# Kernel optimization log

Hardware: AMD Instinct MI355X
Metric: run time of the kernel (lower is better)

## Reference

```python
import jax, jax.numpy as jnp
import numpy as np

NEIGHBOUR_NUM = 8  # args.neighbour_num


def _sqrdis_map(x, y):
    # x: [B,M,3], y: [B,N,3] -> [B,M,N] squared distances
    x2 = jnp.sum(x * x, axis=-1)
    y2 = jnp.sum(y * y, axis=-1)
    inner = jnp.einsum('bmd,bnd->bmn', x, y)
    return x2[:, :, None] + y2[:, None, :] - 2.0 * inner


def _chamfer(x, y):
    d = _sqrdis_map(x, y)
    return d.min(axis=2), d.min(axis=1)


def _neighbor_index(v, k):
    # torch.topk(dist, k+1, largest=False) then drop self
    d = _sqrdis_map(v, v)
    idx = jax.lax.top_k(-d, k + 1)[1]  # ascending distance order
    return idx[:, :, 1:]


def _arap(idx, dp, sp):
    B = dp.shape[0]
    bid = jnp.arange(B)[:, None, None]
    dn = dp[bid, idx] - dp[:, :, None, :]  # [B,N,K,3]
    sn = sp[bid, idx] - sp[:, :, None, :]
    dd = jnp.sqrt(jnp.sum(dn * dn, axis=-1) + 1e-5)
    sd = jnp.sqrt(jnp.sum(sn * sn, axis=-1) + 1e-5)
    diff = dd - sd
    return jnp.sum(diff * diff) / B


def setup_inputs() -> dict:
    key = jax.random.key(0)
    ks = jax.random.split(key, 7)
    T, B, N = 3, 4, 4096
    return {
        'phi': jax.random.normal(ks[0], (T, B, 1024), dtype=jnp.float32),
        'point_weight': jax.random.normal(ks[1], (T, B, N, 1), dtype=jnp.float32),
        'deform_rigid_points': 0.5 * jax.random.normal(ks[2], (T, B, N, 3), dtype=jnp.float32),
        'deformation_points': 0.5 * jax.random.normal(ks[3], (T, B, N, 3), dtype=jnp.float32),
        'rigid_matrix': 0.1 * jax.random.normal(ks[4], (T, B, 4, 4), dtype=jnp.float32),
        'source_points': jax.random.uniform(ks[5], (B, N, 3), dtype=jnp.float32, minval=-1.0, maxval=1.0),
        'target_points': jax.random.uniform(ks[6], (B, N, 3), dtype=jnp.float32, minval=-1.0, maxval=1.0),
    }


def reference(phi, point_weight, deform_rigid_points, deformation_points,
              rigid_matrix, source_points, target_points):
    B = source_points.shape[0]
    T = phi.shape[0]  # iter_time = len(phi_list)
    idx = _neighbor_index(source_points, NEIGHBOUR_NUM)
    trans_mask = jnp.zeros((4, 4), dtype=rigid_matrix.dtype).at[0:3, 3].set(1.0)
    total = jnp.asarray(0.0, dtype=source_points.dtype)
    for t in range(T):  # small fixed iter count, structurally distinct stages
        dp = deformation_points[t]
        # loss_on_cd
        d1, d2 = _chamfer(dp, target_points)
        cd = (jnp.sum(d1) + jnp.sum(d2)) * 0.5 / B
        # loss_on_pd (rigid-deformed vs full deformation)
        diff = deform_rigid_points[t] - dp
        pd = jnp.sum(diff * diff) / B
        # loss_on_sparse
        sp = jnp.mean(jnp.abs(point_weight[t]))
        # loss_on_tran
        tr = trans_mask[None] * rigid_matrix[t]
        tran = jnp.sum(tr * tr) / B
        # loss_on_arap
        ar = _arap(idx, dp, source_points)
        total = total + cd + pd + sp + tran + ar
    return total
```

## Files before the change

kernel.cpp:

```cpp
#include <hip/hip_runtime.h>

#define T_ 3
#define B_ 4
#define N_ 4096
#define K_ 8

#define KNN_BLOCKS (B_ * (N_ / 16))
#define CH_CCH     32
#define CH_CHSZ    (N_ / CH_CCH)
#define CH_CQ      8
#define CH_BLOCKS  (T_ * B_ * 2 * 2 * CH_CCH)

template <int NW>
__device__ inline float block_reduce(float v, float* scratch) {
    #pragma unroll
    for (int off = 32; off > 0; off >>= 1) v += __shfl_down(v, off, 64);
    const int lane = threadIdx.x & 63, wid = threadIdx.x >> 6;
    if (lane == 0) scratch[wid] = v;
    __syncthreads();
    float s = 0.f;
    if (threadIdx.x == 0) {
        #pragma unroll
        for (int w = 0; w < NW; ++w) s += scratch[w];
    }
    return s;
}

#define CE_(A, i, j) { unsigned lo_ = min(A[i], A[j]); A[j] = max(A[i], A[j]); A[i] = lo_; }
__device__ inline void sort8(unsigned s[8]) {
    CE_(s,0,1) CE_(s,2,3) CE_(s,4,5) CE_(s,6,7)
    CE_(s,0,2) CE_(s,1,3) CE_(s,4,6) CE_(s,5,7)
    CE_(s,1,2) CE_(s,5,6)
    CE_(s,0,4) CE_(s,1,5) CE_(s,2,6) CE_(s,3,7)
    CE_(s,2,4) CE_(s,3,5)
    CE_(s,1,2) CE_(s,3,4) CE_(s,5,6)
}
__device__ inline void merge_top8(unsigned a[8], const unsigned s[8]) {
    #pragma unroll
    for (int i = 0; i < 8; ++i) a[i] = min(a[i], s[7 - i]);
    CE_(a,0,4) CE_(a,1,5) CE_(a,2,6) CE_(a,3,7)
    CE_(a,0,2) CE_(a,1,3) CE_(a,4,6) CE_(a,5,7)
    CE_(a,0,1) CE_(a,2,3) CE_(a,4,5) CE_(a,6,7)
}

#define KWIN 1024

__global__ __launch_bounds__(256, 6) void mega_kernel(const float* __restrict__ src,
                                                      const float* __restrict__ dp_all,
                                                      const float* __restrict__ tp,
                                                      int* __restrict__ idx,
                                                      float* __restrict__ pmin,
                                                      float* __restrict__ out) {
    __shared__ unsigned smem_u[4352];
    if (blockIdx.x == 0 && threadIdx.x == 0) *out = 0.f;

    if (blockIdx.x < KNN_BLOCKS) {
        float4* win = (float4*)smem_u;
        const int b  = blockIdx.x / (N_ / 16);
        const int q0 = (blockIdx.x % (N_ / 16)) * 16;
        const float* sb = src + (size_t)b * N_ * 3;

        const int qp = threadIdx.x >> 5;
        const int c  = threadIdx.x & 31;
        const int i0 = q0 + 2 * qp, i1 = i0 + 1;
        const float qx0 = sb[3 * i0], qy0 = sb[3 * i0 + 1], qz0 = sb[3 * i0 + 2];
        const float qx1 = sb[3 * i1], qy1 = sb[3 * i1 + 1], qz1 = sb[3 * i1 + 2];
        const float q20 = fmaf(qx0, qx0, fmaf(qy0, qy0, qz0 * qz0));
        const float q21 = fmaf(qx1, qx1, fmaf(qy1, qy1, qz1 * qz1));

        unsigned a0[K_], a1[K_];
        #pragma unroll
        for (int p = 0; p < K_; ++p) { a0[p] = 0xFFFFFFFFu; a1[p] = 0xFFFFFFFFu; }

        for (int w = 0; w < N_ / KWIN; ++w) {
            __syncthreads();
            for (int j = threadIdx.x; j < KWIN; j += 256) {
                int jg = w * KWIN + j;
                float x = sb[3 * jg], y = sb[3 * jg + 1], z = sb[3 * jg + 2];
                win[j] = make_float4(-2.f * x, -2.f * y, -2.f * z,
                                     fmaf(x, x, fmaf(y, y, z * z)));
            }
            __syncthreads();

            #pragma unroll
            for (int bt = 0; bt < KWIN / 8 / 32; ++bt) {
                unsigned s0[8], s1[8];
                #pragma unroll
                for (int u = 0; u < 8; ++u) {
                    int jl = 32 * (bt * 8 + u) + c;
                    float4 cd = win[jl];
                    int jglob = w * KWIN + jl;
                    float d0 = fmaf(qx0, cd.x, fmaf(qy0, cd.y, fmaf(qz0, cd.z, cd.w))) + q20;
                    float d1 = fmaf(qx1, cd.x, fmaf(qy1, cd.y, fmaf(qz1, cd.z, cd.w))) + q21;
                    unsigned p0 = (__float_as_uint(d0) & 0xFFFFF000u) | (unsigned)jglob;
                    unsigned p1 = (__float_as_uint(d1) & 0xFFFFF000u) | (unsigned)jglob;
                    s0[u] = (jglob == i0) ? 0xFFFFFFFFu : p0;
                    s1[u] = (jglob == i1) ? 0xFFFFFFFFu : p1;
                }
                sort8(s0); merge_top8(a0, s0);
                sort8(s1); merge_top8(a1, s1);
            }
        }
        __syncthreads();

        unsigned* sm = smem_u;
        for (int half = 16; half >= 1; half >>= 1) {
            #pragma unroll
            for (int e = 0; e < K_; ++e) {
                sm[(e * 32 + c) * 17 + 2 * qp]     = a0[e];
                sm[(e * 32 + c) * 17 + 2 * qp + 1] = a1[e];
            }
            __syncthreads();
            if (c < half) {
                unsigned t0[8], t1[8];
                #pragma unroll
                for (int e = 0; e < K_; ++e) {
                    t0[e] = sm[(e * 32 + c + half) * 17 + 2 * qp];
                    t1[e] = sm[(e * 32 + c + half) * 17 + 2 * qp + 1];
                }
                merge_top8(a0, t0);
                merge_top8(a1, t1);
            }
            __syncthreads();
        }

        if (c == 0) {
            int* op0 = idx + ((size_t)b * N_ + i0) * K_;
            int* op1 = idx + ((size_t)b * N_ + i1) * K_;
            #pragma unroll
            for (int k = 0; k < K_; ++k) {
                op0[k] = (int)(a0[k] & 0xFFFu);
                op1[k] = (int)(a1[k] & 0xFFFu);
            }
        }
    } else {
        float4* pts = (float4*)smem_u;
        int blk = blockIdx.x - KNN_BLOCKS;
        const int cc = blk & (CH_CCH - 1); blk >>= 5;
        const int qc = blk & 1;            blk >>= 1;
        const int tbd = blk;
        const int dir = tbd & 1;
        const int tb  = tbd >> 1;
        const int b = tb % B_, t = tb / B_;

        const float* dpb = dp_all + ((size_t)(t * B_ + b)) * N_ * 3;
        const float* tpb = tp + (size_t)b * N_ * 3;
        const float* dbase = dir ? dpb : tpb;
        const float* qbase = dir ? tpb : dpb;

        if (threadIdx.x < CH_CHSZ) {
            int jg = cc * CH_CHSZ + threadIdx.x;
            float x = dbase[3 * jg], y = dbase[3 * jg + 1], z = dbase[3 * jg + 2];
            pts[threadIdx.x] = make_float4(-2.f * x, -2.f * y, -2.f * z,
                                           fmaf(x, x, fmaf(y, y, z * z)));
        }
        __syncthreads();

        float qx[CH_CQ], qy[CH_CQ], qz[CH_CQ], m[CH_CQ];
        #pragma unroll
        for (int u = 0; u < CH_CQ; ++u) {
            int q = qc * 2048 + u * 256 + threadIdx.x;
            qx[u] = qbase[3 * q]; qy[u] = qbase[3 * q + 1]; qz[u] = qbase[3 * q + 2];
            m[u] = 3.4e38f;
        }
        #pragma unroll 2
        for (int j = 0; j < CH_CHSZ; ++j) {
            float4 cd = pts[j];
            #pragma unroll
            for (int u = 0; u < CH_CQ; ++u)
                m[u] = fminf(m[u], fmaf(qx[u], cd.x, fmaf(qy[u], cd.y, fmaf(qz[u], cd.z, cd.w))));
        }
        float* pm = pmin + ((size_t)tbd * CH_CCH + cc) * N_ + qc * 2048;
        #pragma unroll
        for (int u = 0; u < CH_CQ; ++u)
            pm[u * 256 + threadIdx.x] = m[u];
    }
}

__global__ __launch_bounds__(256) void finalize_kernel(const float* __restrict__ dp_all,
                                                       const float* __restrict__ tp,
                                                       const float* __restrict__ src,
                                                       const int* __restrict__ idx,
                                                       const float* __restrict__ pmin,
                                                       const float* __restrict__ drp,
                                                       const float* __restrict__ pw,
                                                       const float* __restrict__ rm,
                                                       float* __restrict__ out) {
    __shared__ float red[4];
    const int blk = blockIdx.x;

    if (blk < 384) {
        const int tbd = blk >> 4;
        const int q = (blk & 15) * 256 + threadIdx.x;
        const int dir = tbd & 1, tb = tbd >> 1, b = tb % B_, t = tb / B_;
        const float* qbase = dir ? tp + (size_t)b * N_ * 3
                                 : dp_all + ((size_t)(t * B_ + b)) * N_ * 3;
        float mrel = 3.4e38f;
        #pragma unroll
        for (int cc = 0; cc < CH_CCH; ++cc)
            mrel = fminf(mrel, pmin[((size_t)tbd * CH_CCH + cc) * N_ + q]);
        float x = qbase[3 * q], y = qbase[3 * q + 1], z = qbase[3 * q + 2];
        float v = fmaf(x, x, fmaf(y, y, z * z)) + mrel;
        float s = block_reduce<4>(v, red);
        if (threadIdx.x == 0) atomicAdd(out, s * (0.5f / B_));
    } else if (blk < 576) {
        const int ab = blk - 384;
        const int chunk = ab & 15;
        const int tb = ab >> 4;
        const int b = tb % B_, t = tb / B_;
        const int n = chunk * 256 + threadIdx.x;
        const float* dp = dp_all + ((size_t)t * B_ + b) * (N_ * 3);
        const float* sp = src + (size_t)b * (N_ * 3);
        const float px = dp[n * 3], py = dp[n * 3 + 1], pz = dp[n * 3 + 2];
        const float sx = sp[n * 3], sy = sp[n * 3 + 1], sz = sp[n * 3 + 2];
        const int* ip = idx + ((size_t)b * N_ + n) * K_;
        float acc = 0.f;
        #pragma unroll
        for (int k = 0; k < K_; ++k) {
            int j = ip[k];
            float dx = dp[j * 3] - px, dy = dp[j * 3 + 1] - py, dz = dp[j * 3 + 2] - pz;
            float ex = sp[j * 3] - sx, ey = sp[j * 3 + 1] - sy, ez = sp[j * 3 + 2] - sz;
            float dd = sqrtf(fmaf(dx, dx, fmaf(dy, dy, dz * dz)) + 1e-5f);
            float sd = sqrtf(fmaf(ex, ex, fmaf(ey, ey, ez * ez)) + 1e-5f);
            float df = dd - sd;
            acc = fmaf(df, df, acc);
        }
        float s = block_reduce<4>(acc, red);
        if (threadIdx.x == 0) atomicAdd(out, s * (1.0f / B_));
    } else {
        const int PD_N = T_ * B_ * N_ * 3;
        const int SP_N = T_ * B_ * N_;
        const int stride = 32 * 256;
        const int gid = (blk - 576) * 256 + threadIdx.x;
        float apd = 0.f;
        for (int i = gid; i < PD_N; i += stride) {
            float d = drp[i] - dp_all[i];
            apd = fmaf(d, d, apd);
        }
        float asp = 0.f;
        for (int i = gid; i < SP_N; i += stride) asp += fabsf(pw[i]);
        float atr = 0.f;
        if (gid < T_ * B_ * 3) {
            int t = gid / (B_ * 3);
            int b = (gid / 3) % B_;
            int r = gid % 3;
            float v = rm[t * B_ * 16 + b * 16 + r * 4 + 3];
            atr = v * v;
        }
        float acc = apd * (1.0f / B_) + asp * (1.0f / (B_ * N_)) + atr * (1.0f / B_);
        float s = block_reduce<4>(acc, red);
        if (threadIdx.x == 0) atomicAdd(out, s);
    }
}

extern "C" void kernel_launch(void* const* d_in, const int* in_sizes, int n_in,
                              void* d_out, int out_size, void* d_ws, size_t ws_size,
                              hipStream_t stream) {
    const float* pw  = (const float*)d_in[1];
    const float* drp = (const float*)d_in[2];
    const float* dp  = (const float*)d_in[3];
    const float* rm  = (const float*)d_in[4];
    const float* sp  = (const float*)d_in[5];
    const float* tp  = (const float*)d_in[6];
    float* out = (float*)d_out;

    int*   idx  = (int*)d_ws;
    float* pmin = (float*)((char*)d_ws + (size_t)B_ * N_ * K_ * 4);

    mega_kernel<<<KNN_BLOCKS + CH_BLOCKS, 256, 0, stream>>>(sp, dp, tp, idx, pmin, out);
    finalize_kernel<<<608, 256, 0, stream>>>(dp, tp, sp, idx, pmin, drp, pw, rm, out);
}
```

Baseline: 131.3 us.

## Compute chamfer min-distances with bf16 split-precision MFMA and drop partial-min buffer

Chamfer nearest-distance work now runs on matrix cores. The coordinates are split into bf16 high and low parts so the 16x16x32 MFMA emits near-fp32 squared-distance terms, and each block keeps a running min over all candidate windows. Because every block scans all candidates, the per-chunk partial-min buffer and its finalize reduction pass go away. The output is zeroed with a memset instead of inside the kernel, and the launch-bounds occupancy hint drops from 6 to 4. The hi/lo bf16 split risks small precision loss and puts more register pressure on the KNN path, which shares the kernel.

```diff
diff --git a/kernel.cpp b/kernel.cpp
--- a/kernel.cpp
+++ b/kernel.cpp
@@ -6,10 +6,12 @@
 #define K_ 8
 
 #define KNN_BLOCKS (B_ * (N_ / 16))
-#define CH_CCH     32
-#define CH_CHSZ    (N_ / CH_CCH)
-#define CH_CQ      8
-#define CH_BLOCKS  (T_ * B_ * 2 * 2 * CH_CCH)
+#define CH_BLOCKS  (T_ * B_ * 2 * 16)
+#define KWIN 1024
+#define CWIN 512
+
+typedef short bf16x8 __attribute__((ext_vector_type(8)));
+typedef float f32x4  __attribute__((ext_vector_type(4)));
 
 template <int NW>
 __device__ inline float block_reduce(float v, float* scratch) {
@@ -43,19 +45,24 @@
     CE_(a,0,1) CE_(a,2,3) CE_(a,4,5) CE_(a,6,7)
 }
 
-#define KWIN 1024
-
-__global__ __launch_bounds__(256, 6) void mega_kernel(const float* __restrict__ src,
+__device__ inline short hi16(float v) { return (short)(__float_as_uint(v) >> 16); }
+__device__ inline float residual(float v) {
+    return v - __uint_as_float(__float_as_uint(v) & 0xFFFF0000u);
+}
+__device__ inline unsigned pk2(short a, short b) {
+    return (unsigned)(unsigned short)a | ((unsigned)(unsigned short)b << 16);
+}
+#define BF16_ONE ((short)0x3F80)
+
+__global__ __launch_bounds__(256, 4) void mega_kernel(const float* __restrict__ src,
                                                       const float* __restrict__ dp_all,
                                                       const float* __restrict__ tp,
                                                       int* __restrict__ idx,
-                                                      float* __restrict__ pmin,
                                                       float* __restrict__ out) {
-    __shared__ unsigned smem_u[4352];
-    if (blockIdx.x == 0 && threadIdx.x == 0) *out = 0.f;
+    __shared__ uint4 smem4[1088];
 
     if (blockIdx.x < KNN_BLOCKS) {
-        float4* win = (float4*)smem_u;
+        float4* win = (float4*)smem4;
         const int b  = blockIdx.x / (N_ / 16);
         const int q0 = (blockIdx.x % (N_ / 16)) * 16;
         const float* sb = src + (size_t)b * N_ * 3;
@@ -103,7 +110,7 @@
         }
         __syncthreads();
 
-        unsigned* sm = smem_u;
+        unsigned* sm = (unsigned*)smem4;
         for (int half = 16; half >= 1; half >>= 1) {
             #pragma unroll
             for (int e = 0; e < K_; ++e) {
@@ -134,54 +141,98 @@
             }
         }
     } else {
-        float4* pts = (float4*)smem_u;
-        int blk = blockIdx.x - KNN_BLOCKS;
-        const int cc = blk & (CH_CCH - 1); blk >>= 5;
-        const int qc = blk & 1;            blk >>= 1;
-        const int tbd = blk;
+        uint4* alds = smem4;
+        const int cb   = blockIdx.x - KNN_BLOCKS;
+        const int tbd  = cb >> 4;
+        const int slab = cb & 15;
         const int dir = tbd & 1;
         const int tb  = tbd >> 1;
         const int b = tb % B_, t = tb / B_;
 
         const float* dpb = dp_all + ((size_t)(t * B_ + b)) * N_ * 3;
         const float* tpb = tp + (size_t)b * N_ * 3;
-        const float* dbase = dir ? dpb : tpb;
+        const float* cbase = dir ? dpb : tpb;
         const float* qbase = dir ? tpb : dpb;
 
-        if (threadIdx.x < CH_CHSZ) {
-            int jg = cc * CH_CHSZ + threadIdx.x;
-            float x = dbase[3 * jg], y = dbase[3 * jg + 1], z = dbase[3 * jg + 2];
-            pts[threadIdx.x] = make_float4(-2.f * x, -2.f * y, -2.f * z,
-                                           fmaf(x, x, fmaf(y, y, z * z)));
+        const int lane = threadIdx.x & 63;
+        const int wave = threadIdx.x >> 6;
+        const int quad = lane >> 4;
+        const int n    = lane & 15;
+
+        bf16x8 bfrag[4];
+        float  q2r[4];
+        #pragma unroll
+        for (int s = 0; s < 4; ++s) {
+            int qid = slab * 256 + wave * 64 + s * 16 + n;
+            float x = qbase[3 * qid], y = qbase[3 * qid + 1], z = qbase[3 * qid + 2];
+            q2r[s] = fmaf(x, x, fmaf(y, y, z * z));
+            short hx = hi16(x), hy = hi16(y), hz = hi16(z);
+            short lx = hi16(residual(x)), ly = hi16(residual(y)), lz = hi16(residual(z));
+            if (quad == 0)
+                bfrag[s] = (bf16x8){hx, hy, hz, hx, hy, hz, BF16_ONE, BF16_ONE};
+            else if (quad == 1)
+                bfrag[s] = (bf16x8){lx, ly, lz, lx, ly, lz, 0, 0};
+            else
+                bfrag[s] = (bf16x8)(short)0;
+        }
+
+        float run[4] = {3.4e38f, 3.4e38f, 3.4e38f, 3.4e38f};
+        const f32x4 zero4 = {0.f, 0.f, 0.f, 0.f};
+
+        for (int w = 0; w < N_ / CWIN; ++w) {
+            __syncthreads();
+            #pragma unroll
+            for (int r = 0; r < 2; ++r) {
+                int jloc = threadIdx.x * 2 + r;
+                int jg = w * CWIN + jloc;
+                float x = cbase[3 * jg], y = cbase[3 * jg + 1], z = cbase[3 * jg + 2];
+                float p2 = fmaf(x, x, fmaf(y, y, z * z));
+                float mx = -2.f * x, my = -2.f * y, mz = -2.f * z;
+                short mhx = hi16(mx), mhy = hi16(my), mhz = hi16(mz);
+                short mlx = hi16(residual(mx)), mly = hi16(residual(my)), mlz = hi16(residual(mz));
+                short p2h = hi16(p2), p2l = hi16(residual(p2));
+                uint4 f0 = make_uint4(pk2(mhx, mhy), pk2(mhz, mlx), pk2(mly, mlz), pk2(p2h, p2l));
+                uint4 f1 = make_uint4(f0.x, f0.y, f0.z, 0u);
+                int tile = jloc >> 4, m = jloc & 15;
+                alds[tile * 32 + m]      = f0;
+                alds[tile * 32 + 16 + m] = f1;
+            }
+            __syncthreads();
+
+            #pragma unroll 4
+            for (int tile = 0; tile < CWIN / 16; ++tile) {
+                bf16x8 af = (bf16x8)(short)0;
+                if (quad < 2) {
+                    union { uint4 u; bf16x8 v; } cv;
+                    cv.u = alds[tile * 32 + quad * 16 + n];
+                    af = cv.v;
+                }
+                #pragma unroll
+                for (int s = 0; s < 4; ++s) {
+                    f32x4 d = __builtin_amdgcn_mfma_f32_16x16x32_bf16(af, bfrag[s], zero4, 0, 0, 0);
+                    float r3 = fminf(fminf(d[0], d[1]), d[2]);
+                    run[s] = fminf(fminf(run[s], r3), d[3]);
+                }
+            }
+        }
+
+        float vsum = 0.f;
+        #pragma unroll
+        for (int s = 0; s < 4; ++s) {
+            float r = run[s];
+            r = fminf(r, __shfl_xor(r, 32));
+            r = fminf(r, __shfl_xor(r, 16));
+            if (lane < 16) vsum += r + q2r[s];
         }
         __syncthreads();
-
-        float qx[CH_CQ], qy[CH_CQ], qz[CH_CQ], m[CH_CQ];
-        #pragma unroll
-        for (int u = 0; u < CH_CQ; ++u) {
-            int q = qc * 2048 + u * 256 + threadIdx.x;
-            qx[u] = qbase[3 * q]; qy[u] = qbase[3 * q + 1]; qz[u] = qbase[3 * q + 2];
-            m[u] = 3.4e38f;
-        }
-        #pragma unroll 2
-        for (int j = 0; j < CH_CHSZ; ++j) {
-            float4 cd = pts[j];
-            #pragma unroll
-            for (int u = 0; u < CH_CQ; ++u)
-                m[u] = fminf(m[u], fmaf(qx[u], cd.x, fmaf(qy[u], cd.y, fmaf(qz[u], cd.z, cd.w))));
-        }
-        float* pm = pmin + ((size_t)tbd * CH_CCH + cc) * N_ + qc * 2048;
-        #pragma unroll
-        for (int u = 0; u < CH_CQ; ++u)
-            pm[u * 256 + threadIdx.x] = m[u];
+        float ssum = block_reduce<4>(vsum, (float*)smem4);
+        if (threadIdx.x == 0) atomicAdd(out, ssum * (0.5f / B_));
     }
 }
 
 __global__ __launch_bounds__(256) void finalize_kernel(const float* __restrict__ dp_all,
-                                                       const float* __restrict__ tp,
                                                        const float* __restrict__ src,
                                                        const int* __restrict__ idx,
-                                                       const float* __restrict__ pmin,
                                                        const float* __restrict__ drp,
                                                        const float* __restrict__ pw,
                                                        const float* __restrict__ rm,
@@ -189,24 +240,9 @@
     __shared__ float red[4];
     const int blk = blockIdx.x;
 
-    if (blk < 384) {
-        const int tbd = blk >> 4;
-        const int q = (blk & 15) * 256 + threadIdx.x;
-        const int dir = tbd & 1, tb = tbd >> 1, b = tb % B_, t = tb / B_;
-        const float* qbase = dir ? tp + (size_t)b * N_ * 3
-                                 : dp_all + ((size_t)(t * B_ + b)) * N_ * 3;
-        float mrel = 3.4e38f;
-        #pragma unroll
-        for (int cc = 0; cc < CH_CCH; ++cc)
-            mrel = fminf(mrel, pmin[((size_t)tbd * CH_CCH + cc) * N_ + q]);
-        float x = qbase[3 * q], y = qbase[3 * q + 1], z = qbase[3 * q + 2];
-        float v = fmaf(x, x, fmaf(y, y, z * z)) + mrel;
-        float s = block_reduce<4>(v, red);
-        if (threadIdx.x == 0) atomicAdd(out, s * (0.5f / B_));
-    } else if (blk < 576) {
-        const int ab = blk - 384;
-        const int chunk = ab & 15;
-        const int tb = ab >> 4;
+    if (blk < 192) {
+        const int chunk = blk & 15;
+        const int tb = blk >> 4;
         const int b = tb % B_, t = tb / B_;
         const int n = chunk * 256 + threadIdx.x;
         const float* dp = dp_all + ((size_t)t * B_ + b) * (N_ * 3);
@@ -231,7 +267,7 @@
         const int PD_N = T_ * B_ * N_ * 3;
         const int SP_N = T_ * B_ * N_;
         const int stride = 32 * 256;
-        const int gid = (blk - 576) * 256 + threadIdx.x;
+        const int gid = (blk - 192) * 256 + threadIdx.x;
         float apd = 0.f;
         for (int i = gid; i < PD_N; i += stride) {
             float d = drp[i] - dp_all[i];
@@ -264,9 +300,9 @@
     const float* tp  = (const float*)d_in[6];
     float* out = (float*)d_out;
 
-    int*   idx  = (int*)d_ws;
-    float* pmin = (float*)((char*)d_ws + (size_t)B_ * N_ * K_ * 4);
-
-    mega_kernel<<<KNN_BLOCKS + CH_BLOCKS, 256, 0, stream>>>(sp, dp, tp, idx, pmin, out);
-    finalize_kernel<<<608, 256, 0, stream>>>(dp, tp, sp, idx, pmin, drp, pw, rm, out);
-}
+    int* idx = (int*)d_ws;
+
+    hipMemsetAsync(out, 0, sizeof(float), stream);
+    mega_kernel<<<KNN_BLOCKS + CH_BLOCKS, 256, 0, stream>>>(sp, dp, tp, idx, out);
+    finalize_kernel<<<224, 256, 0, stream>>>(dp, sp, idx, drp, pw, rm, out);
+}
```

New measurement: 133.2 us. About the same (+1.4%).
